# Kernel tuning notes

Measured on AMD Instinct MI355X. Metric: run time of the kernel, lower is better.

## Reference

```python
import jax, jax.numpy as jnp
import numpy as np

THRESH = 0.5   # spike_args['thresh']
LENS = 0.5     # spike_args['lens'] (surrogate gradient window)
DECAY = 0.2    # spike_args['decay']
XISHUSPIKE = 0.5
XISHUADA = 0.2

@jax.custom_vjp
def spike_fn(v):
    return (v > THRESH).astype(v.dtype)

def _spike_fwd(v):
    return spike_fn(v), v

def _spike_bwd(v, g):
    # rectangular surrogate: pass grad where |v - thresh| < lens
    return (g * (jnp.abs(v - THRESH) < LENS).astype(g.dtype),)

spike_fn.defvjp(_spike_fwd, _spike_bwd)

def setup_inputs() -> dict:
    key = jax.random.key(0)
    k1, k2, k3, k4 = jax.random.split(key, 4)
    B, IN, OUT = 512, 2048, 2048
    x = jax.random.normal(k1, (B, IN), jnp.float32)
    W_fc = jax.random.normal(k2, (OUT, IN), jnp.float32) / np.sqrt(IN).astype(np.float32)
    b_fc = jnp.zeros((OUT,), jnp.float32)
    W_rec = jax.random.normal(k3, (OUT, OUT), jnp.float32) / np.sqrt(OUT).astype(np.float32)
    b_rec = jnp.zeros((OUT,), jnp.float32)
    eye = jnp.eye(OUT, dtype=jnp.int32)
    keep = jax.random.bernoulli(k4, 0.5, (OUT, OUT)).astype(jnp.int32)
    rec_mask = (1 - eye) * keep
    return {"x": x, "W_fc": W_fc, "b_fc": b_fc, "W_rec": W_rec,
            "b_rec": b_rec, "rec_mask": rec_mask, "spike_window": 16}

def reference(x, W_fc, b_fc, W_rec, b_rec, rec_mask, spike_window):
    # feed-forward drive is constant across the time loop (same x each step, noise off)
    ff = x @ W_fc.T + b_fc                      # [B, OUT]
    Wr = W_rec * rec_mask.astype(W_rec.dtype)    # masked recurrent weight (idempotent)
    z = jnp.zeros_like(ff)

    def step(carry, _):
        mem, spk, ath, ssum = carry
        ath = 0.9 * ath + XISHUSPIKE * spk
        mem_ff = mem * DECAY * (1.0 - spk) + ff - ath * XISHUADA
        s_ff = spike_fn(mem_ff)
        mem_r = spk @ Wr.T + b_rec
        s_r = spike_fn(mem_r)
        mem = mem_ff + mem_r
        spk = s_ff + s_r
        ssum = ssum + spk
        return (mem, spk, ath, ssum), None

    (mem, spk, ath, ssum), _ = jax.lax.scan(step, (z, z, z, z), None, length=spike_window)
    return ssum
```

## Files before the change

### kernel.cpp

```cpp
#include <hip/hip_runtime.h>


#pragma clang fp contract(off)

#define B_ROWS 512
#define N_OUT 2048
#define K_IN 2048
#define NSTEP 16
#define NPANEL 4
#define PANK 512
#define BKT 16
#define BTM 32
#define BTN 256
#define WTM 8
#define NJ 4
#define NTILES (PANK / BKT)

typedef const __attribute__((address_space(1))) void* gptr_t;
typedef __attribute__((address_space(3))) void* lptr_t;

__global__ __launch_bounds__(256) void transpose_tile(
    const float* __restrict__ W, const int* __restrict__ mask,
    float* __restrict__ WT, int useMask)
{
    __shared__ float t[32][33];
    int kb = blockIdx.x * 32, nb = blockIdx.y * 32;
    int tx = threadIdx.x, ty = threadIdx.y;
#pragma unroll
    for (int r = 0; r < 32; r += 8) {
        size_t src = (size_t)(nb + ty + r) * K_IN + (kb + tx);
        float v = W[src];
        if (useMask) v *= (float)mask[src];
        t[ty + r][tx] = v;
    }
    __syncthreads();
#pragma unroll
    for (int r = 0; r < 32; r += 8)
        WT[(size_t)(kb + ty + r) * N_OUT + (nb + tx)] = t[tx][ty + r];
}

__global__ __launch_bounds__(256) void init_state(float* mem, float* ath,
                                                  float* ssum, float* spk) {
    int idx = blockIdx.x * 256 + threadIdx.x;
    mem[idx] = 0.0f; ath[idx] = 0.0f; ssum[idx] = 0.0f; spk[idx] = 0.0f;
}

__global__ __launch_bounds__(256, 2) void gemm_panel(
    const float* __restrict__ A,
    const float* __restrict__ BT,
    float* __restrict__ Cp)
{
    __shared__ float Bs[2][BKT][BTN];
    __shared__ float As[2][BKT][BTM];
    const int tid  = threadIdx.x;
    const int w    = tid >> 6;
    const int lane = tid & 63;
    const int n0 = blockIdx.x * BTN;
    const int m0 = blockIdx.y * BTM;
    const int pan = blockIdx.z;
    const int kbase = pan * PANK;

    float acc[WTM][NJ];
#pragma unroll
    for (int m = 0; m < WTM; m++)
#pragma unroll
        for (int j = 0; j < NJ; j++) acc[m][j] = 0.0f;

    auto stage = [&](int buf, int kt) {
#pragma unroll
        for (int i = 0; i < 4; i++) {
            const int row = w * 4 + i;
            __builtin_amdgcn_global_load_lds(
                (gptr_t)(uintptr_t)(BT + (size_t)(kbase + kt * BKT + row) * N_OUT
                                        + n0 + lane * 4),
                (lptr_t)(uintptr_t)&Bs[buf][row][0], 16, 0, 0);
        }
#pragma unroll
        for (int i = 0; i < 2; i++) {
            const int j = w * 2 + i;
            __builtin_amdgcn_global_load_lds(
                (gptr_t)(uintptr_t)(A + (size_t)(m0 + (lane & 31)) * K_IN
                                       + kbase + kt * BKT + 2 * j + (lane >> 5)),
                (lptr_t)(uintptr_t)&As[buf][2 * j][0], 4, 0, 0);
        }
    };

    stage(0, 0);
    for (int kt = 0; kt < NTILES; kt++) {
        const int buf = kt & 1;
        __syncthreads();
        if (kt + 1 < NTILES) stage(buf ^ 1, kt + 1);

        float4 bC  = *(const float4*)&Bs[buf][0][lane * 4];
        float4 aC0 = *(const float4*)&As[buf][0][w * WTM];
        float4 aC1 = *(const float4*)&As[buf][0][w * WTM + 4];
#pragma unroll
        for (int kk = 0; kk < BKT; kk++) {
            float4 bN, aN0, aN1;
            if (kk + 1 < BKT) {
                bN  = *(const float4*)&Bs[buf][kk + 1][lane * 4];
                aN0 = *(const float4*)&As[buf][kk + 1][w * WTM];
                aN1 = *(const float4*)&As[buf][kk + 1][w * WTM + 4];
            }
            float a[WTM] = {aC0.x, aC0.y, aC0.z, aC0.w,
                            aC1.x, aC1.y, aC1.z, aC1.w};
            float b[NJ] = {bC.x, bC.y, bC.z, bC.w};
#pragma unroll
            for (int m = 0; m < WTM; m++)
#pragma unroll
                for (int j = 0; j < NJ; j++)
                    acc[m][j] = fmaf(a[m], b[j], acc[m][j]);
            if (kk + 1 < BKT) { bC = bN; aC0 = aN0; aC1 = aN1; }
        }
    }

    const size_t P = (size_t)B_ROWS * N_OUT;
#pragma unroll
    for (int m = 0; m < WTM; m++) {
        size_t off = (size_t)pan * P
                   + (size_t)(m0 + w * WTM + m) * N_OUT + n0 + lane * NJ;
        *(float4*)(Cp + off) = make_float4(acc[m][0], acc[m][1], acc[m][2], acc[m][3]);
    }
}

__global__ __launch_bounds__(256) void ff_fold(
    const float* __restrict__ Cp, const float* __restrict__ b_fc,
    float* __restrict__ ff)
{
    const size_t P = (size_t)B_ROWS * N_OUT;
    size_t base = ((size_t)blockIdx.x * 256 + threadIdx.x) * 4;
    int n = (int)(base & (N_OUT - 1));
    float4 p0 = *(const float4*)(Cp + base);
    float4 p1 = *(const float4*)(Cp + P + base);
    float4 p2 = *(const float4*)(Cp + 2 * P + base);
    float4 p3 = *(const float4*)(Cp + 3 * P + base);
    float4 bv = *(const float4*)(b_fc + n);
    float4 o;
    o.x = (((p0.x + p1.x) + p2.x) + p3.x) + bv.x;
    o.y = (((p0.y + p1.y) + p2.y) + p3.y) + bv.y;
    o.z = (((p0.z + p1.z) + p2.z) + p3.z) + bv.z;
    o.w = (((p0.w + p1.w) + p2.w) + p3.w) + bv.w;
    *(float4*)(ff + base) = o;
}

__global__ __launch_bounds__(256) void fold_update(
    const float* __restrict__ Cp, const float* __restrict__ b_rec,
    const float* __restrict__ spk_in, const float* __restrict__ ff,
    float* __restrict__ mem, float* __restrict__ ath,
    float* __restrict__ ssum, float* __restrict__ spk_out,
    float* __restrict__ out, int last)
{
    const size_t P = (size_t)B_ROWS * N_OUT;
    size_t base = ((size_t)blockIdx.x * 256 + threadIdx.x) * 4;
    int n = (int)(base & (N_OUT - 1));
    float4 p0 = *(const float4*)(Cp + base);
    float4 p1 = *(const float4*)(Cp + P + base);
    float4 p2 = *(const float4*)(Cp + 2 * P + base);
    float4 p3 = *(const float4*)(Cp + 3 * P + base);
    float4 bv = *(const float4*)(b_rec + n);
    float4 sv = *(const float4*)(spk_in + base);
    float4 av = *(const float4*)(ath + base);
    float4 mv = *(const float4*)(mem + base);
    float4 fv = *(const float4*)(ff + base);
    float4 uv = *(const float4*)(ssum + base);

    float cr[4] = {(((p0.x + p1.x) + p2.x) + p3.x),
                   (((p0.y + p1.y) + p2.y) + p3.y),
                   (((p0.z + p1.z) + p2.z) + p3.z),
                   (((p0.w + p1.w) + p2.w) + p3.w)};
    float ba[4] = {bv.x, bv.y, bv.z, bv.w};
    float sa[4] = {sv.x, sv.y, sv.z, sv.w};
    float aa[4] = {av.x, av.y, av.z, av.w};
    float ma[4] = {mv.x, mv.y, mv.z, mv.w};
    float fa[4] = {fv.x, fv.y, fv.z, fv.w};
    float ua[4] = {uv.x, uv.y, uv.z, uv.w};
    float mo[4], ao[4], uo[4], so[4];
#pragma unroll
    for (int j = 0; j < 4; j++) {
        float memr  = cr[j] + ba[j];
        float sp    = sa[j];
        float t1    = aa[j] * 0.9f;
        float t2    = 0.5f * sp;
        float athn  = t1 + t2;
        float u1    = ma[j] * 0.2f;
        float u2    = 1.0f - sp;
        float u3    = u1 * u2;
        float u4    = u3 + fa[j];
        float u5    = athn * 0.2f;
        float memff = u4 - u5;
        float s_ff  = (memff > 0.5f) ? 1.0f : 0.0f;
        float s_r   = (memr  > 0.5f) ? 1.0f : 0.0f;
        mo[j] = memff + memr;
        ao[j] = athn;
        so[j] = s_ff + s_r;
        uo[j] = ua[j] + so[j];
    }
    *(float4*)(mem + base)     = make_float4(mo[0], mo[1], mo[2], mo[3]);
    *(float4*)(ath + base)     = make_float4(ao[0], ao[1], ao[2], ao[3]);
    *(float4*)(ssum + base)    = make_float4(uo[0], uo[1], uo[2], uo[3]);
    *(float4*)(spk_out + base) = make_float4(so[0], so[1], so[2], so[3]);
    if (last)
        *(float4*)(out + base) = make_float4(uo[0], uo[1], uo[2], uo[3]);
}

extern "C" void kernel_launch(void* const* d_in, const int* in_sizes, int n_in,
                              void* d_out, int out_size, void* d_ws, size_t ws_size,
                              hipStream_t stream) {
    const float* x      = (const float*)d_in[0];
    const float* W_fc   = (const float*)d_in[1];
    const float* b_fc   = (const float*)d_in[2];
    const float* W_rec  = (const float*)d_in[3];
    const float* b_rec  = (const float*)d_in[4];
    const int*   rmask  = (const int*)d_in[5];

    char* ws = (char*)d_ws;
    float* WT   = (float*)(ws);
    float* ff   = (float*)(ws + (16u << 20));
    float* mem  = (float*)(ws + (20u << 20));
    float* ath  = (float*)(ws + (24u << 20));
    float* ssum = (float*)(ws + (28u << 20));
    float* spkA = (float*)(ws + (32u << 20));
    float* spkB = (float*)(ws + (36u << 20));
    float* Cp   = (float*)(ws + (40u << 20));

    dim3 gridT(K_IN / 32, N_OUT / 32);
    dim3 blkT(32, 8);
    dim3 gridS((B_ROWS * N_OUT) / 256);
    dim3 gridG(N_OUT / BTN, B_ROWS / BTM, NPANEL);
    dim3 gridF((B_ROWS * N_OUT) / (256 * 4));

    transpose_tile<<<gridT, blkT, 0, stream>>>(W_fc, rmask, WT, 0);
    init_state<<<gridS, 256, 0, stream>>>(mem, ath, ssum, spkA);
    gemm_panel<<<gridG, 256, 0, stream>>>(x, WT, Cp);
    ff_fold<<<gridF, 256, 0, stream>>>(Cp, b_fc, ff);
    transpose_tile<<<gridT, blkT, 0, stream>>>(W_rec, rmask, WT, 1);

    for (int t = 0; t < NSTEP; t++) {
        const float* si = (t & 1) ? spkB : spkA;
        float*       so = (t & 1) ? spkA : spkB;
        gemm_panel<<<gridG, 256, 0, stream>>>(si, WT, Cp);
        fold_update<<<gridF, 256, 0, stream>>>(
            Cp, b_rec, si, ff, mem, ath, ssum, so, (float*)d_out, t == NSTEP - 1);
    }
}
```

Measured before the change: 1.172 ms.

## Load A operand into registers and broadcast via readlane instead of LDS

The gemm_panel kernel no longer stages the A tile through shared memory. Each lane now loads A values straight from global memory into registers, prefetching one K-tile ahead, and the per-row values are broadcast across the wave with readlane so they act as scalar operands in the FMAs. The B operand loads from LDS are prefetched two steps ahead with a three-slot ring instead of one step ahead. This removes the LDS traffic and LDS space for A, but adds uncoalesced strided global loads and many readlane instructions in the inner loop.

```diff
diff --git a/kernel.cpp b/kernel.cpp
--- a/kernel.cpp
+++ b/kernel.cpp
@@ -51,7 +51,6 @@
     float* __restrict__ Cp)
 {
     __shared__ float Bs[2][BKT][BTN];
-    __shared__ float As[2][BKT][BTM];
     const int tid  = threadIdx.x;
     const int w    = tid >> 6;
     const int lane = tid & 63;
@@ -75,15 +74,12 @@
                                         + n0 + lane * 4),
                 (lptr_t)(uintptr_t)&Bs[buf][row][0], 16, 0, 0);
         }
-#pragma unroll
-        for (int i = 0; i < 2; i++) {
-            const int j = w * 2 + i;
-            __builtin_amdgcn_global_load_lds(
-                (gptr_t)(uintptr_t)(A + (size_t)(m0 + (lane & 31)) * K_IN
-                                       + kbase + kt * BKT + 2 * j + (lane >> 5)),
-                (lptr_t)(uintptr_t)&As[buf][2 * j][0], 4, 0, 0);
-        }
     };
+
+    const float* aSrc = A + (size_t)(m0 + w * WTM + (lane & 7)) * K_IN
+                          + kbase + (lane >> 3);
+    float aC0 = aSrc[0];
+    float aC1 = aSrc[8];
 
     stage(0, 0);
     for (int kt = 0; kt < NTILES; kt++) {
@@ -91,27 +87,33 @@
         __syncthreads();
         if (kt + 1 < NTILES) stage(buf ^ 1, kt + 1);
 
-        float4 bC  = *(const float4*)&Bs[buf][0][lane * 4];
-        float4 aC0 = *(const float4*)&As[buf][0][w * WTM];
-        float4 aC1 = *(const float4*)&As[buf][0][w * WTM + 4];
+        float aN0, aN1;
+        if (kt + 1 < NTILES) {
+            aN0 = aSrc[(kt + 1) * BKT];
+            aN1 = aSrc[(kt + 1) * BKT + 8];
+        }
+
+        float4 bset[3];
+        bset[0] = *(const float4*)&Bs[buf][0][lane * 4];
+        bset[1] = *(const float4*)&Bs[buf][1][lane * 4];
 #pragma unroll
         for (int kk = 0; kk < BKT; kk++) {
-            float4 bN, aN0, aN1;
-            if (kk + 1 < BKT) {
-                bN  = *(const float4*)&Bs[buf][kk + 1][lane * 4];
-                aN0 = *(const float4*)&As[buf][kk + 1][w * WTM];
-                aN1 = *(const float4*)&As[buf][kk + 1][w * WTM + 4];
+            if (kk + 2 < BKT)
+                bset[(kk + 2) % 3] = *(const float4*)&Bs[buf][kk + 2][lane * 4];
+            const float4 b4 = bset[kk % 3];
+            const float b[NJ] = {b4.x, b4.y, b4.z, b4.w};
+            const float aHold = (kk < 8) ? aC0 : aC1;
+            const int   kbit  = (kk & 7) * 8;
+#pragma unroll
+            for (int m = 0; m < WTM; m++) {
+                const float am = __int_as_float(
+                    __builtin_amdgcn_readlane(__float_as_int(aHold), kbit + m));
+#pragma unroll
+                for (int j = 0; j < NJ; j++)
+                    acc[m][j] = fmaf(am, b[j], acc[m][j]);
             }
-            float a[WTM] = {aC0.x, aC0.y, aC0.z, aC0.w,
-                            aC1.x, aC1.y, aC1.z, aC1.w};
-            float b[NJ] = {bC.x, bC.y, bC.z, bC.w};
-#pragma unroll
-            for (int m = 0; m < WTM; m++)
-#pragma unroll
-                for (int j = 0; j < NJ; j++)
-                    acc[m][j] = fmaf(a[m], b[j], acc[m][j]);
-            if (kk + 1 < BKT) { bC = bN; aC0 = aN0; aC1 = aN1; }
         }
+        if (kt + 1 < NTILES) { aC0 = aN0; aC1 = aN1; }
     }
 
     const size_t P = (size_t)B_ROWS * N_OUT;
```

Result: slower. 1.422 ms (+21.4%).
